# Optimization experiments

Measured on AMD Instinct MI355X. Metric: run time of the kernel, lower is better.

Reference implementation:

```python
import jax, jax.numpy as jnp
import numpy as np
import math

B, S, HID = 16, 512, 768
NUM_LABELS = 9
NUM_HEADS = 4
HEAD_DIM = HID // NUM_HEADS
MAX_REL = 5
B_PERSON = 1
I_PERSON = 2
LN_EPS = 1e-5


def setup_inputs() -> dict:
    key = jax.random.key(0)
    ks = jax.random.split(key, 16)
    w = lambda k, shp: jax.random.normal(k, shp, dtype=jnp.float32) * 0.02
    return {
        "sequence_output": jax.random.normal(ks[0], (B, S, HID), dtype=jnp.float32),
        "Wq": w(ks[1], (HID, HID)), "bq": jnp.zeros((HID,), jnp.float32),
        "Wk": w(ks[2], (HID, HID)), "bk": jnp.zeros((HID,), jnp.float32),
        "Wv": w(ks[3], (HID, HID)), "bv": jnp.zeros((HID,), jnp.float32),
        "Wo": w(ks[4], (HID, HID)), "bo": jnp.zeros((HID,), jnp.float32),
        "ln_g": jnp.ones((HID,), jnp.float32), "ln_b": jnp.zeros((HID,), jnp.float32),
        "Ws": w(ks[5], (HID, NUM_LABELS)), "bs": jnp.zeros((NUM_LABELS,), jnp.float32),
        "entity_bias": w(ks[6], (NUM_LABELS,)),
    }


def _heads(x):
    # [B,S,HID] -> [B,H,S,D]
    return x.reshape(B, S, NUM_HEADS, HEAD_DIM).transpose(0, 2, 1, 3)


def reference(sequence_output, Wq, bq, Wk, bk, Wv, bv, Wo, bo, ln_g, ln_b, Ws, bs, entity_bias):
    x = sequence_output
    q = _heads(x @ Wq + bq)
    k = _heads(x @ Wk + bk)
    v = _heads(x @ Wv + bv)

    scores = jnp.einsum("bhqd,bhkd->bhqk", q, k)
    # relative position bias: exp(-0.1 * clamp(|i-j|, 0, MAX_REL)), broadcast over b,h
    idx = jnp.arange(S, dtype=jnp.float32)
    dist = jnp.abs(idx[None, :] - idx[:, None])  # [S,S]
    rel_bias = jnp.exp(-0.1 * jnp.clip(dist, 0.0, float(MAX_REL)))
    dist_mask = -0.1 * dist
    scores = (scores + rel_bias) / math.sqrt(HEAD_DIM) + dist_mask
    probs = jax.nn.softmax(scores, axis=-1)  # dropout is identity in eval

    ctx = jnp.einsum("bhqk,bhkd->bhqd", probs, v)
    ctx = ctx.transpose(0, 2, 1, 3).reshape(B, S, HID)
    out = ctx @ Wo + bo

    h = x + out
    mu = jnp.mean(h, axis=-1, keepdims=True)
    var = jnp.mean(jnp.square(h - mu), axis=-1, keepdims=True)
    h = (h - mu) * jax.lax.rsqrt(var + LN_EPS) * ln_g + ln_b

    span_logits = h @ Ws + bs  # [B,S,L]
    # vectorized entity-bias post-process: the torch loop adds entity_bias[I_PERSON]
    # TWICE to final_logits[:, j, I_PERSON] whenever argmax(span_logits[:, j-1]) == B_PERSON
    prev_is_b = jnp.argmax(span_logits[:, :-1], axis=-1) == B_PERSON  # [B,S-1]
    bump = jnp.where(prev_is_b, 2.0 * entity_bias[I_PERSON], 0.0)
    final_logits = span_logits.at[:, 1:, I_PERSON].add(bump)
    return final_logits
```

## Files before the change

kernel.cpp:

```cpp
#include <hip/hip_runtime.h>
#include <math.h>

#define SEQ 512
#define HID 768
#define NBATCH 16
#define ROWS 8192
#define INV_SQRT_D 0.07216878364870323f

typedef short s8v __attribute__((ext_vector_type(8)));
typedef _Float16 h8v __attribute__((ext_vector_type(8)));
typedef float f4v __attribute__((ext_vector_type(4)));
typedef unsigned short u16;

__device__ __forceinline__ u16 f2h(float f) {
  _Float16 h = (_Float16)f;
  return __builtin_bit_cast(u16, h);
}

template <int KSTEPS>
__device__ __forceinline__ void mm_core128(
    const u16* __restrict__ A, const int lda,
    const u16* __restrict__ B, const int ldb,
    u16* lds, f4v (&acc)[4][4])
{
  const int tid = threadIdx.x;
  const int w = tid >> 6, ln = tid & 63;
  const u16* src = (w >> 1) ? B : A;
  const int ld = (w >> 1) ? ldb : lda;
  const int half = w & 1;
  const int srow = ln >> 2;
  const int csw  = ((ln & 3) - (ln >> 3)) & 3;
  const int ml = ln & 15, quad = ln >> 4;
  const int fo2 = ((quad + ((ln >> 1) & 3)) & 3) * 8;
  const int wr = (w >> 1) * 64, wc = (w & 1) * 64;

  const u16* gp[4];
  int lpo[4];
#pragma unroll
  for (int t = 0; t < 4; ++t) {
    const int row = half * 64 + t * 16 + srow;
    gp[t]  = src + (size_t)row * ld + csw * 8;
    lpo[t] = (w >> 1) * 4096 + half * 2048 + t * 512 + ln * 8;
  }
  s8v c[8];
#pragma unroll
  for (int t = 0; t < 4; ++t) {
    c[t]     = *(const s8v*)gp[t];
    c[4 + t] = *(const s8v*)(gp[t] + 32);
  }

  for (int kp = 0; kp < KSTEPS / 2; ++kp) {
    __syncthreads();
#pragma unroll
    for (int t = 0; t < 4; ++t) {
      *(s8v*)&lds[lpo[t]]        = c[t];
      *(s8v*)&lds[8192 + lpo[t]] = c[4 + t];
    }
    __syncthreads();
    if (kp + 1 < KSTEPS / 2) {
      const int k0 = (kp + 1) * 64;
#pragma unroll
      for (int t = 0; t < 4; ++t) {
        c[t]     = *(const s8v*)(gp[t] + k0);
        c[4 + t] = *(const s8v*)(gp[t] + k0 + 32);
      }
    }
#pragma unroll
    for (int sub = 0; sub < 2; ++sub) {
      const int so = sub * 8192;
      h8v a[4], b[4];
#pragma unroll
      for (int i = 0; i < 4; ++i)
        a[i] = *(const h8v*)&lds[so + (wr + i * 16 + ml) * 32 + fo2];
#pragma unroll
      for (int j = 0; j < 4; ++j)
        b[j] = *(const h8v*)&lds[so + 4096 + (wc + j * 16 + ml) * 32 + fo2];
#pragma unroll
      for (int i = 0; i < 4; ++i)
#pragma unroll
        for (int j = 0; j < 4; ++j)
          acc[i][j] = __builtin_amdgcn_mfma_f32_16x16x32_f16(a[i], b[j], acc[i][j], 0, 0, 0);
    }
  }
}

__global__ __launch_bounds__(256) void splitx(const float* __restrict__ x,
                                              u16* __restrict__ xh)
{
  const int i = blockIdx.x * 256 + threadIdx.x;
  const float4 v = ((const float4*)x)[i];
  ((ushort4*)xh)[i] = make_ushort4(f2h(v.x), f2h(v.y), f2h(v.z), f2h(v.w));
}

__global__ __launch_bounds__(256) void wsplit(
    const float* __restrict__ Wq, const float* __restrict__ Wk,
    const float* __restrict__ Wv, const float* __restrict__ Wo,
    u16* __restrict__ WTh)
{
  __shared__ float t[32][33];
  const int z = blockIdx.z;
  const float* W = (z == 0) ? Wq : (z == 1) ? Wk : (z == 2) ? Wv : Wo;
  const int n0 = blockIdx.x * 32, k0 = blockIdx.y * 32;
  const int tx = threadIdx.x & 31, ty = threadIdx.x >> 5;
#pragma unroll
  for (int i = 0; i < 4; ++i)
    t[ty + 8 * i][tx] = W[(size_t)(k0 + ty + 8 * i) * HID + n0 + tx];
  __syncthreads();
#pragma unroll
  for (int i = 0; i < 4; ++i) {
    const float v = t[tx][ty + 8 * i];
    const size_t idx = (size_t)z * HID * HID + (size_t)(n0 + ty + 8 * i) * HID + k0 + tx;
    WTh[idx] = f2h(v);
  }
}

__global__ __launch_bounds__(256, 3) void qkv_mm(
    const u16* __restrict__ xh, const u16* __restrict__ WTh,
    const float* __restrict__ bq, const float* __restrict__ bk, const float* __restrict__ bv,
    u16* __restrict__ qh, u16* __restrict__ kh, u16* __restrict__ vtmp16)
{
  __shared__ u16 lds[16384];
  const int id = blockIdx.x;
  const int xcd = id & 7;
  const int s = id >> 3;
  const int bx = s % 6;
  const int yl = (s / 6) & 7;
  const int z  = s / 48;
  const int bm = (yl * 8 + xcd) * 128;
  const int bn = bx * 128;
  const size_t wtoff = (size_t)z * HID * HID + (size_t)bn * HID;
  f4v acc[4][4];
#pragma unroll
  for (int i = 0; i < 4; ++i)
#pragma unroll
    for (int j = 0; j < 4; ++j) acc[i][j] = (f4v)0.f;
  mm_core128<24>(xh + (size_t)bm * HID, HID, WTh + wtoff, HID, lds, acc);
  const int tid = threadIdx.x, w = tid >> 6, ln = tid & 63;
  const int ml = ln & 15, quad = ln >> 4;
  const int wr = (w >> 1) * 64, wc = (w & 1) * 64;
  const float* bias = (z == 0) ? bq : (z == 1) ? bk : bv;
#pragma unroll
  for (int i = 0; i < 4; ++i)
#pragma unroll
    for (int j = 0; j < 4; ++j) {
      const int gcol = bn + wc + j * 16 + ml;
      const float bv_ = bias[gcol];
#pragma unroll
      for (int r = 0; r < 4; ++r) {
        const int grow = bm + wr + i * 16 + quad * 4 + r;
        const float v = acc[i][j][r] + bv_;
        const size_t idx = (size_t)grow * HID + gcol;
        if (z == 2)      vtmp16[idx] = f2h(v);
        else if (z == 0) qh[idx] = f2h(v);
        else             kh[idx] = f2h(v);
      }
    }
}

__global__ __launch_bounds__(256) void vtrans(const u16* __restrict__ vtmp16,
                                              u16* __restrict__ vTh)
{
  __shared__ u16 t[32][33];
  const int b = blockIdx.z, n0 = blockIdx.x * 32, c0 = blockIdx.y * 32;
  const int tx = threadIdx.x & 31, ty = threadIdx.x >> 5;
  const u16* src = vtmp16 + (size_t)b * SEQ * HID;
#pragma unroll
  for (int i = 0; i < 4; ++i)
    t[ty + 8 * i][tx] = src[(size_t)(c0 + ty + 8 * i) * HID + n0 + tx];
  __syncthreads();
#pragma unroll
  for (int i = 0; i < 4; ++i) {
    const size_t idx = (size_t)b * HID * SEQ + (size_t)(n0 + ty + 8 * i) * SEQ + c0 + tx;
    vTh[idx] = t[tx][ty + 8 * i];
  }
}

__global__ __launch_bounds__(256, 2) void attn_fused(
    const u16* __restrict__ qh, const u16* __restrict__ kh,
    const u16* __restrict__ vTh, u16* __restrict__ ch)
{
  __shared__ u16 lds[22528];
  __shared__ float red[4][32];
  const int z = blockIdx.y, b = z >> 2, hh = z & 3;
  const int bm = blockIdx.x * 32;
  const int tid = threadIdx.x, w = tid >> 6, ln = tid & 63;
  const int ml = ln & 15, quad = ln >> 4;
  const int fo2 = ((quad + ((ml >> 1) & 3)) & 3) * 8;
  const u16* qbase = qh + (size_t)(b * SEQ + bm) * HID + hh * 192;
  const u16* kbase = kh + (size_t)(b * SEQ) * HID + hh * 192;

  const int brow0 = tid >> 2, bsc = tid & 3;
  const u16* bgp[8];
  int blo[8];
#pragma unroll
  for (int t = 0; t < 8; ++t) {
    const int row = t * 64 + brow0;
    const int lc = (bsc - (row >> 1)) & 3;
    bgp[t] = kbase + (size_t)row * HID + lc * 8;
    blo[t] = 1024 + row * 32 + bsc * 8;
  }
  const bool hasA = tid < 128;
  const int arow = tid >> 2;
  const int alc = ((tid & 3) - (arow >> 1)) & 3;
  const u16* agp = qbase + (size_t)arow * HID + alc * 8;
  const int alo = arow * 32 + (tid & 3) * 8;

  s8v ca;
  s8v cb[8];
  if (hasA) ca = *(const s8v*)agp;
#pragma unroll
  for (int t = 0; t < 8; ++t) cb[t] = *(const s8v*)bgp[t];

  f4v acc[2][8];
#pragma unroll
  for (int i = 0; i < 2; ++i)
#pragma unroll
    for (int j = 0; j < 8; ++j) acc[i][j] = (f4v)0.f;

  for (int ks = 0; ks < 6; ++ks) {
    __syncthreads();
    if (hasA) *(s8v*)&lds[alo] = ca;
#pragma unroll
    for (int t = 0; t < 8; ++t) *(s8v*)&lds[blo[t]] = cb[t];
    __syncthreads();
    if (ks + 1 < 6) {
      const int k0 = (ks + 1) * 32;
      if (hasA) ca = *(const s8v*)(agp + k0);
#pragma unroll
      for (int t = 0; t < 8; ++t) cb[t] = *(const s8v*)(bgp[t] + k0);
    }
    h8v a[2];
#pragma unroll
    for (int i = 0; i < 2; ++i)
      a[i] = *(const h8v*)&lds[(i * 16 + ml) * 32 + fo2];
    h8v bfr[8];
#pragma unroll
    for (int j = 0; j < 8; ++j)
      bfr[j] = *(const h8v*)&lds[1024 + (w * 128 + j * 16 + ml) * 32 + fo2];
#pragma unroll
    for (int i = 0; i < 2; ++i)
#pragma unroll
      for (int j = 0; j < 8; ++j)
        acc[i][j] = __builtin_amdgcn_mfma_f32_16x16x32_f16(a[i], bfr[j], acc[i][j], 0, 0, 0);
  }

#pragma unroll
  for (int i = 0; i < 2; ++i)
#pragma unroll
    for (int j = 0; j < 8; ++j) {
      const int scol = w * 128 + j * 16 + ml;
#pragma unroll
      for (int r = 0; r < 4; ++r) {
        const int srow = bm + i * 16 + quad * 4 + r;
        const float dist = fabsf((float)(srow - scol));
        const float rel = __expf(-0.1f * fminf(dist, 5.0f));
        acc[i][j][r] = (acc[i][j][r] + rel) * INV_SQRT_D - 0.1f * dist;
      }
    }

  float mx[2][4];
#pragma unroll
  for (int i = 0; i < 2; ++i)
#pragma unroll
    for (int r = 0; r < 4; ++r) {
      float m = acc[i][0][r];
#pragma unroll
      for (int j = 1; j < 8; ++j) m = fmaxf(m, acc[i][j][r]);
#pragma unroll
      for (int o = 1; o < 16; o <<= 1) m = fmaxf(m, __shfl_xor(m, o, 64));
      mx[i][r] = m;
    }
  if (ml == 0) {
#pragma unroll
    for (int i = 0; i < 2; ++i)
#pragma unroll
      for (int r = 0; r < 4; ++r) red[w][i * 16 + quad * 4 + r] = mx[i][r];
  }
  __syncthreads();
#pragma unroll
  for (int i = 0; i < 2; ++i)
#pragma unroll
    for (int r = 0; r < 4; ++r) {
      const int R = i * 16 + quad * 4 + r;
      mx[i][r] = fmaxf(fmaxf(red[0][R], red[1][R]), fmaxf(red[2][R], red[3][R]));
    }
  __syncthreads();

  float sm[2][4];
#pragma unroll
  for (int i = 0; i < 2; ++i)
#pragma unroll
    for (int r = 0; r < 4; ++r) {
      float s = 0.f;
#pragma unroll
      for (int j = 0; j < 8; ++j) {
        const float p = __expf(acc[i][j][r] - mx[i][r]);
        acc[i][j][r] = p;
        s += p;
      }
#pragma unroll
      for (int o = 1; o < 16; o <<= 1) s += __shfl_xor(s, o, 64);
      sm[i][r] = s;
    }
  if (ml == 0) {
#pragma unroll
    for (int i = 0; i < 2; ++i)
#pragma unroll
      for (int r = 0; r < 4; ++r) red[w][i * 16 + quad * 4 + r] = sm[i][r];
  }
  __syncthreads();
#pragma unroll
  for (int i = 0; i < 2; ++i)
#pragma unroll
    for (int r = 0; r < 4; ++r) {
      const int R = i * 16 + quad * 4 + r;
      mx[i][r] = 1.0f / (red[0][R] + red[1][R] + red[2][R] + red[3][R]);
    }
  __syncthreads();

#pragma unroll
  for (int i = 0; i < 2; ++i)
#pragma unroll
    for (int r = 0; r < 4; ++r) {
      const int row = i * 16 + quad * 4 + r;
      const int rsw = (row >> 1) & 3;
      const int rbase = row * 512;
#pragma unroll
      for (int j = 0; j < 8; ++j) {
        const int col = w * 128 + j * 16 + ml;
        const int addr = rbase + (col & ~31) + ((((col >> 3) & 3) + rsw) & 3) * 8 + (col & 7);
        lds[addr] = f2h(acc[i][j][r] * mx[i][r]);
      }
    }

  const u16* vbase = vTh + (size_t)b * HID * SEQ + (size_t)(hh * 192) * SEQ;
  const u16* vgp[3];
  int vlo[3];
#pragma unroll
  for (int t = 0; t < 3; ++t) {
    const int cch = t * 256 + tid;
    const int vrow = cch >> 2, vsc = cch & 3;
    const int vlc = (vsc - (vrow >> 1)) & 3;
    vgp[t] = vbase + (size_t)vrow * SEQ + vlc * 8;
    vlo[t] = 16384 + cch * 8;
  }
  s8v vc[3];
#pragma unroll
  for (int t = 0; t < 3; ++t) vc[t] = *(const s8v*)vgp[t];

  f4v acc2[2][3];
#pragma unroll
  for (int i = 0; i < 2; ++i)
#pragma unroll
    for (int j = 0; j < 3; ++j) acc2[i][j] = (f4v)0.f;

  for (int ks = 0; ks < 16; ++ks) {
    __syncthreads();
#pragma unroll
    for (int t = 0; t < 3; ++t) *(s8v*)&lds[vlo[t]] = vc[t];
    __syncthreads();
    if (ks + 1 < 16) {
      const int k0 = (ks + 1) * 32;
#pragma unroll
      for (int t = 0; t < 3; ++t) vc[t] = *(const s8v*)(vgp[t] + k0);
    }
    h8v a2[2];
#pragma unroll
    for (int i = 0; i < 2; ++i)
      a2[i] = *(const h8v*)&lds[(i * 16 + ml) * 512 + ks * 32 + fo2];
    h8v b2[3];
#pragma unroll
    for (int j = 0; j < 3; ++j)
      b2[j] = *(const h8v*)&lds[16384 + (w * 48 + j * 16 + ml) * 32 + fo2];
#pragma unroll
    for (int i = 0; i < 2; ++i)
#pragma unroll
      for (int j = 0; j < 3; ++j)
        acc2[i][j] = __builtin_amdgcn_mfma_f32_16x16x32_f16(a2[i], b2[j], acc2[i][j], 0, 0, 0);
  }

#pragma unroll
  for (int i = 0; i < 2; ++i)
#pragma unroll
    for (int j = 0; j < 3; ++j) {
      const int gcol = hh * 192 + w * 48 + j * 16 + ml;
#pragma unroll
      for (int r = 0; r < 4; ++r) {
        const int m = bm + i * 16 + quad * 4 + r;
        ch[(size_t)(b * SEQ + m) * HID + gcol] = f2h(acc2[i][j][r]);
      }
    }
}

__global__ __launch_bounds__(256, 3) void proj_mm(
    const u16* __restrict__ ch, const u16* __restrict__ WTh,
    const float* __restrict__ bo, const float* __restrict__ x, float* __restrict__ h)
{
  __shared__ u16 lds[16384];
  const int id = blockIdx.x;
  const int xcd = id & 7;
  const int s = id >> 3;
  const int bx = s % 6;
  const int yl = s / 6;
  const int bm = (yl * 8 + xcd) * 128;
  const int bn = bx * 128;
  const size_t wtoff = (size_t)3 * HID * HID + (size_t)bn * HID;
  f4v acc[4][4];
#pragma unroll
  for (int i = 0; i < 4; ++i)
#pragma unroll
    for (int j = 0; j < 4; ++j) acc[i][j] = (f4v)0.f;
  mm_core128<24>(ch + (size_t)bm * HID, HID, WTh + wtoff, HID, lds, acc);
  const int tid = threadIdx.x, w = tid >> 6, ln = tid & 63;
  const int ml = ln & 15, quad = ln >> 4;
  const int wr = (w >> 1) * 64, wc = (w & 1) * 64;
#pragma unroll
  for (int i = 0; i < 4; ++i)
#pragma unroll
    for (int j = 0; j < 4; ++j) {
      const int gcol = bn + wc + j * 16 + ml;
      const float bv_ = bo[gcol];
#pragma unroll
      for (int r = 0; r < 4; ++r) {
        const int grow = bm + wr + i * 16 + quad * 4 + r;
        const size_t idx = (size_t)grow * HID + gcol;
        h[idx] = acc[i][j][r] + bv_ + x[idx];
      }
    }
}

__global__ __launch_bounds__(256) void ln_logits_kernel(
    const float* __restrict__ h, const float* __restrict__ g,
    const float* __restrict__ bta, const float* __restrict__ Ws,
    const float* __restrict__ bsv, float* __restrict__ span)
{
  const int row = blockIdx.x;
  const int tid = threadIdx.x;
  const float* hr = h + (size_t)row * HID;
  const float x0 = hr[tid], x1 = hr[tid + 256], x2 = hr[tid + 512];
  float s = x0 + x1 + x2;
  float sq = x0 * x0 + x1 * x1 + x2 * x2;
#pragma unroll
  for (int o = 32; o > 0; o >>= 1) { s += __shfl_down(s, o, 64); sq += __shfl_down(sq, o, 64); }
  __shared__ float red[8];
  __shared__ float smu, srs;
  const int wid = tid >> 6, lid = tid & 63;
  if (lid == 0) { red[wid] = s; red[4 + wid] = sq; }
  __syncthreads();
  if (tid == 0) {
    const float ts = red[0] + red[1] + red[2] + red[3];
    const float tq = red[4] + red[5] + red[6] + red[7];
    const float mu = ts / 768.0f;
    const float var = tq / 768.0f - mu * mu;
    smu = mu; srs = rsqrtf(var + 1e-5f);
  }
  __syncthreads();
  const float mu = smu, rs = srs;
  const float n0 = (x0 - mu) * rs * g[tid] + bta[tid];
  const float n1 = (x1 - mu) * rs * g[tid + 256] + bta[tid + 256];
  const float n2 = (x2 - mu) * rs * g[tid + 512] + bta[tid + 512];
  float pl[9];
#pragma unroll
  for (int l = 0; l < 9; ++l)
    pl[l] = n0 * Ws[(size_t)tid * 9 + l]
          + n1 * Ws[(size_t)(tid + 256) * 9 + l]
          + n2 * Ws[(size_t)(tid + 512) * 9 + l];
#pragma unroll
  for (int l = 0; l < 9; ++l)
#pragma unroll
    for (int o = 32; o > 0; o >>= 1) pl[l] += __shfl_down(pl[l], o, 64);
  __shared__ float lred[4][9];
  if (lid == 0) {
#pragma unroll
    for (int l = 0; l < 9; ++l) lred[wid][l] = pl[l];
  }
  __syncthreads();
  if (tid < 9) {
    span[(size_t)row * 9 + tid] =
        lred[0][tid] + lred[1][tid] + lred[2][tid] + lred[3][tid] + bsv[tid];
  }
}

__global__ __launch_bounds__(256) void bump_kernel(
    const float* __restrict__ span, const float* __restrict__ eb, float* __restrict__ out)
{
  const int idx = blockIdx.x * 256 + threadIdx.x;
  if (idx >= ROWS) return;
  const int j = idx & (SEQ - 1);
  const float* sl = span + (size_t)idx * 9;
  float v[9];
#pragma unroll
  for (int l = 0; l < 9; ++l) v[l] = sl[l];
  if (j >= 1) {
    const float* sp = sl - 9;
    float m = sp[0]; int am = 0;
#pragma unroll
    for (int l = 1; l < 9; ++l) { const float t = sp[l]; if (t > m) { m = t; am = l; } }
    if (am == 1) v[2] += 2.0f * eb[2];
  }
#pragma unroll
  for (int l = 0; l < 9; ++l) out[(size_t)idx * 9 + l] = v[l];
}

extern "C" void kernel_launch(void* const* d_in, const int* in_sizes, int n_in,
                              void* d_out, int out_size, void* d_ws, size_t ws_size,
                              hipStream_t stream)
{
  (void)in_sizes; (void)n_in; (void)out_size; (void)ws_size;
  const float* x   = (const float*)d_in[0];
  const float* Wq  = (const float*)d_in[1];
  const float* bq  = (const float*)d_in[2];
  const float* Wk  = (const float*)d_in[3];
  const float* bk  = (const float*)d_in[4];
  const float* Wv  = (const float*)d_in[5];
  const float* bv  = (const float*)d_in[6];
  const float* Wo  = (const float*)d_in[7];
  const float* bo  = (const float*)d_in[8];
  const float* lng = (const float*)d_in[9];
  const float* lnb = (const float*)d_in[10];
  const float* Ws  = (const float*)d_in[11];
  const float* bs  = (const float*)d_in[12];
  const float* eb  = (const float*)d_in[13];
  float* out = (float*)d_out;

  char* ws = (char*)d_ws;
  u16* xh  = (u16*)(ws + 0);
  u16* vTh = xh;
  u16* WTh = (u16*)(ws + 25165824);
  u16* qh  = (u16*)(ws + 34603008);
  u16* kh  = (u16*)(ws + 59768832);
  u16* vtmp16 = (u16*)(ws + 84934656);
  float* hb = (float*)(ws + 84934656);
  float* spanb = (float*)(ws + 152043520);
  u16* ctxh = qh;

  splitx<<<dim3(1572864 / 256), 256, 0, stream>>>(x, xh);
  wsplit<<<dim3(24, 24, 4), 256, 0, stream>>>(Wq, Wk, Wv, Wo, WTh);
  qkv_mm<<<dim3(1152), 256, 0, stream>>>(xh, WTh, bq, bk, bv, qh, kh, vtmp16);
  vtrans<<<dim3(24, 16, 16), 256, 0, stream>>>(vtmp16, vTh);
  attn_fused<<<dim3(16, 64), 256, 0, stream>>>(qh, kh, vTh, ctxh);
  proj_mm<<<dim3(384), 256, 0, stream>>>(ctxh, WTh, bo, x, hb);
  ln_logits_kernel<<<dim3(ROWS), 256, 0, stream>>>(hb, lng, lnb, Ws, bs, spanb);
  bump_kernel<<<dim3(ROWS / 256), 256, 0, stream>>>(spanb, eb, out);
}
```

Measured before the change: 240.5 us.

## Load attention operands straight from global memory and drop the softmax max pass

The attention kernel no longer stages Q, K and V tiles through shared memory with double-buffered copies and barriers. Each wave now loads its MFMA fragments directly from global memory, which works because the waves do not share K or V fragments. Softmax skips the row-max reduction and its barriers, and normalisation by the row sum moves to the output store. Shared memory shrinks, occupancy is raised to 4 blocks, the P buffer rows are padded to 520, and blocks are remapped so each XCD handles whole batch-head groups. Dropping the max subtraction assumes scores stay small enough for exp not to overflow, and the direct fragment loads are narrower and less coalesced than the old staged copies.

```diff
diff --git a/kernel.cpp b/kernel.cpp
--- a/kernel.cpp
+++ b/kernel.cpp
@@ -175,41 +175,32 @@
   }
 }
 
-__global__ __launch_bounds__(256, 2) void attn_fused(
+__global__ __launch_bounds__(256, 4) void attn_fused(
     const u16* __restrict__ qh, const u16* __restrict__ kh,
     const u16* __restrict__ vTh, u16* __restrict__ ch)
 {
-  __shared__ u16 lds[22528];
+  __shared__ u16 lds[16640];
   __shared__ float red[4][32];
-  const int z = blockIdx.y, b = z >> 2, hh = z & 3;
-  const int bm = blockIdx.x * 32;
+  const int f = blockIdx.x;
+  const int xcd = f & 7, s = f >> 3;
+  const int z = xcd * 8 + (s >> 4);
+  const int bm = (s & 15) * 32;
+  const int b = z >> 2, hh = z & 3;
   const int tid = threadIdx.x, w = tid >> 6, ln = tid & 63;
   const int ml = ln & 15, quad = ln >> 4;
   const int fo2 = ((quad + ((ml >> 1) & 3)) & 3) * 8;
+
   const u16* qbase = qh + (size_t)(b * SEQ + bm) * HID + hh * 192;
-  const u16* kbase = kh + (size_t)(b * SEQ) * HID + hh * 192;
-
-  const int brow0 = tid >> 2, bsc = tid & 3;
-  const u16* bgp[8];
-  int blo[8];
-#pragma unroll
-  for (int t = 0; t < 8; ++t) {
-    const int row = t * 64 + brow0;
-    const int lc = (bsc - (row >> 1)) & 3;
-    bgp[t] = kbase + (size_t)row * HID + lc * 8;
-    blo[t] = 1024 + row * 32 + bsc * 8;
-  }
-  const bool hasA = tid < 128;
-  const int arow = tid >> 2;
-  const int alc = ((tid & 3) - (arow >> 1)) & 3;
-  const u16* agp = qbase + (size_t)arow * HID + alc * 8;
-  const int alo = arow * 32 + (tid & 3) * 8;
-
-  s8v ca;
-  s8v cb[8];
-  if (hasA) ca = *(const s8v*)agp;
-#pragma unroll
-  for (int t = 0; t < 8; ++t) cb[t] = *(const s8v*)bgp[t];
+  const u16* kbase = kh + (size_t)b * SEQ * HID + hh * 192;
+
+  const u16* qp[2];
+#pragma unroll
+  for (int i = 0; i < 2; ++i)
+    qp[i] = qbase + (size_t)(i * 16 + ml) * HID + quad * 8;
+  const u16* kp[8];
+#pragma unroll
+  for (int j = 0; j < 8; ++j)
+    kp[j] = kbase + (size_t)(w * 128 + j * 16 + ml) * HID + quad * 8;
 
   f4v acc[2][8];
 #pragma unroll
@@ -217,33 +208,31 @@
 #pragma unroll
     for (int j = 0; j < 8; ++j) acc[i][j] = (f4v)0.f;
 
+#pragma unroll
   for (int ks = 0; ks < 6; ++ks) {
-    __syncthreads();
-    if (hasA) *(s8v*)&lds[alo] = ca;
-#pragma unroll
-    for (int t = 0; t < 8; ++t) *(s8v*)&lds[blo[t]] = cb[t];
-    __syncthreads();
-    if (ks + 1 < 6) {
-      const int k0 = (ks + 1) * 32;
-      if (hasA) ca = *(const s8v*)(agp + k0);
-#pragma unroll
-      for (int t = 0; t < 8; ++t) cb[t] = *(const s8v*)(bgp[t] + k0);
-    }
+    const int ko = ks * 32;
     h8v a[2];
 #pragma unroll
-    for (int i = 0; i < 2; ++i)
-      a[i] = *(const h8v*)&lds[(i * 16 + ml) * 32 + fo2];
-    h8v bfr[8];
-#pragma unroll
-    for (int j = 0; j < 8; ++j)
-      bfr[j] = *(const h8v*)&lds[1024 + (w * 128 + j * 16 + ml) * 32 + fo2];
-#pragma unroll
-    for (int i = 0; i < 2; ++i)
-#pragma unroll
-      for (int j = 0; j < 8; ++j)
-        acc[i][j] = __builtin_amdgcn_mfma_f32_16x16x32_f16(a[i], bfr[j], acc[i][j], 0, 0, 0);
-  }
-
+    for (int i = 0; i < 2; ++i) a[i] = *(const h8v*)(qp[i] + ko);
+#pragma unroll
+    for (int jh = 0; jh < 2; ++jh) {
+      h8v bf[4];
+#pragma unroll
+      for (int j = 0; j < 4; ++j) bf[j] = *(const h8v*)(kp[jh * 4 + j] + ko);
+#pragma unroll
+      for (int i = 0; i < 2; ++i)
+#pragma unroll
+        for (int j = 0; j < 4; ++j)
+          acc[i][jh * 4 + j] =
+              __builtin_amdgcn_mfma_f32_16x16x32_f16(a[i], bf[j], acc[i][jh * 4 + j], 0, 0, 0);
+    }
+  }
+
+  float sm[2][4];
+#pragma unroll
+  for (int i = 0; i < 2; ++i)
+#pragma unroll
+    for (int r = 0; r < 4; ++r) sm[i][r] = 0.f;
 #pragma unroll
   for (int i = 0; i < 2; ++i)
 #pragma unroll
@@ -252,71 +241,28 @@
 #pragma unroll
       for (int r = 0; r < 4; ++r) {
         const int srow = bm + i * 16 + quad * 4 + r;
-        const float dist = fabsf((float)(srow - scol));
-        const float rel = __expf(-0.1f * fminf(dist, 5.0f));
-        acc[i][j][r] = (acc[i][j][r] + rel) * INV_SQRT_D - 0.1f * dist;
-      }
-    }
-
-  float mx[2][4];
+        const float fd = fabsf((float)(srow - scol));
+        const float rel = __expf(-0.1f * fminf(fd, 5.0f));
+        const float p = __expf((acc[i][j][r] + rel) * INV_SQRT_D - 0.1f * fd);
+        acc[i][j][r] = p;
+        sm[i][r] += p;
+      }
+    }
 #pragma unroll
   for (int i = 0; i < 2; ++i)
 #pragma unroll
     for (int r = 0; r < 4; ++r) {
-      float m = acc[i][0][r];
-#pragma unroll
-      for (int j = 1; j < 8; ++j) m = fmaxf(m, acc[i][j][r]);
-#pragma unroll
-      for (int o = 1; o < 16; o <<= 1) m = fmaxf(m, __shfl_xor(m, o, 64));
-      mx[i][r] = m;
+      float t = sm[i][r];
+#pragma unroll
+      for (int o = 1; o < 16; o <<= 1) t += __shfl_xor(t, o, 64);
+      sm[i][r] = t;
     }
   if (ml == 0) {
 #pragma unroll
     for (int i = 0; i < 2; ++i)
 #pragma unroll
-      for (int r = 0; r < 4; ++r) red[w][i * 16 + quad * 4 + r] = mx[i][r];
-  }
-  __syncthreads();
-#pragma unroll
-  for (int i = 0; i < 2; ++i)
-#pragma unroll
-    for (int r = 0; r < 4; ++r) {
-      const int R = i * 16 + quad * 4 + r;
-      mx[i][r] = fmaxf(fmaxf(red[0][R], red[1][R]), fmaxf(red[2][R], red[3][R]));
-    }
-  __syncthreads();
-
-  float sm[2][4];
-#pragma unroll
-  for (int i = 0; i < 2; ++i)
-#pragma unroll
-    for (int r = 0; r < 4; ++r) {
-      float s = 0.f;
-#pragma unroll
-      for (int j = 0; j < 8; ++j) {
-        const float p = __expf(acc[i][j][r] - mx[i][r]);
-        acc[i][j][r] = p;
-        s += p;
-      }
-#pragma unroll
-      for (int o = 1; o < 16; o <<= 1) s += __shfl_xor(s, o, 64);
-      sm[i][r] = s;
-    }
-  if (ml == 0) {
-#pragma unroll
-    for (int i = 0; i < 2; ++i)
-#pragma unroll
       for (int r = 0; r < 4; ++r) red[w][i * 16 + quad * 4 + r] = sm[i][r];
   }
-  __syncthreads();
-#pragma unroll
-  for (int i = 0; i < 2; ++i)
-#pragma unroll
-    for (int r = 0; r < 4; ++r) {
-      const int R = i * 16 + quad * 4 + r;
-      mx[i][r] = 1.0f / (red[0][R] + red[1][R] + red[2][R] + red[3][R]);
-    }
-  __syncthreads();
 
 #pragma unroll
   for (int i = 0; i < 2; ++i)
@@ -324,29 +270,30 @@
     for (int r = 0; r < 4; ++r) {
       const int row = i * 16 + quad * 4 + r;
       const int rsw = (row >> 1) & 3;
-      const int rbase = row * 512;
+      const int rbase = row * 520;
 #pragma unroll
       for (int j = 0; j < 8; ++j) {
         const int col = w * 128 + j * 16 + ml;
         const int addr = rbase + (col & ~31) + ((((col >> 3) & 3) + rsw) & 3) * 8 + (col & 7);
-        lds[addr] = f2h(acc[i][j][r] * mx[i][r]);
-      }
+        lds[addr] = f2h(acc[i][j][r]);
+      }
+    }
+  __syncthreads();
+
+  float isum[2][4];
+#pragma unroll
+  for (int i = 0; i < 2; ++i)
+#pragma unroll
+    for (int r = 0; r < 4; ++r) {
+      const int R = i * 16 + quad * 4 + r;
+      isum[i][r] = 1.0f / (red[0][R] + red[1][R] + red[2][R] + red[3][R]);
     }
 
   const u16* vbase = vTh + (size_t)b * HID * SEQ + (size_t)(hh * 192) * SEQ;
-  const u16* vgp[3];
-  int vlo[3];
-#pragma unroll
-  for (int t = 0; t < 3; ++t) {
-    const int cch = t * 256 + tid;
-    const int vrow = cch >> 2, vsc = cch & 3;
-    const int vlc = (vsc - (vrow >> 1)) & 3;
-    vgp[t] = vbase + (size_t)vrow * SEQ + vlc * 8;
-    vlo[t] = 16384 + cch * 8;
-  }
-  s8v vc[3];
-#pragma unroll
-  for (int t = 0; t < 3; ++t) vc[t] = *(const s8v*)vgp[t];
+  const u16* vp[3];
+#pragma unroll
+  for (int j = 0; j < 3; ++j)
+    vp[j] = vbase + (size_t)(w * 48 + j * 16 + ml) * SEQ + quad * 8;
 
   f4v acc2[2][3];
 #pragma unroll
@@ -354,24 +301,15 @@
 #pragma unroll
     for (int j = 0; j < 3; ++j) acc2[i][j] = (f4v)0.f;
 
+#pragma unroll
   for (int ks = 0; ks < 16; ++ks) {
-    __syncthreads();
-#pragma unroll
-    for (int t = 0; t < 3; ++t) *(s8v*)&lds[vlo[t]] = vc[t];
-    __syncthreads();
-    if (ks + 1 < 16) {
-      const int k0 = (ks + 1) * 32;
-#pragma unroll
-      for (int t = 0; t < 3; ++t) vc[t] = *(const s8v*)(vgp[t] + k0);
-    }
     h8v a2[2];
 #pragma unroll
     for (int i = 0; i < 2; ++i)
-      a2[i] = *(const h8v*)&lds[(i * 16 + ml) * 512 + ks * 32 + fo2];
+      a2[i] = *(const h8v*)&lds[(i * 16 + ml) * 520 + ks * 32 + fo2];
     h8v b2[3];
 #pragma unroll
-    for (int j = 0; j < 3; ++j)
-      b2[j] = *(const h8v*)&lds[16384 + (w * 48 + j * 16 + ml) * 32 + fo2];
+    for (int j = 0; j < 3; ++j) b2[j] = *(const h8v*)(vp[j] + ks * 32);
 #pragma unroll
     for (int i = 0; i < 2; ++i)
 #pragma unroll
@@ -387,7 +325,7 @@
 #pragma unroll
       for (int r = 0; r < 4; ++r) {
         const int m = bm + i * 16 + quad * 4 + r;
-        ch[(size_t)(b * SEQ + m) * HID + gcol] = f2h(acc2[i][j][r]);
+        ch[(size_t)(b * SEQ + m) * HID + gcol] = f2h(acc2[i][j][r] * isum[i][r]);
       }
     }
 }
@@ -538,7 +476,7 @@
   wsplit<<<dim3(24, 24, 4), 256, 0, stream>>>(Wq, Wk, Wv, Wo, WTh);
   qkv_mm<<<dim3(1152), 256, 0, stream>>>(xh, WTh, bq, bk, bv, qh, kh, vtmp16);
   vtrans<<<dim3(24, 16, 16), 256, 0, stream>>>(vtmp16, vTh);
-  attn_fused<<<dim3(16, 64), 256, 0, stream>>>(qh, kh, vTh, ctxh);
+  attn_fused<<<dim3(1024), 256, 0, stream>>>(qh, kh, vTh, ctxh);
   proj_mm<<<dim3(384), 256, 0, stream>>>(ctxh, WTh, bo, x, hb);
   ln_logits_kernel<<<dim3(ROWS), 256, 0, stream>>>(hb, lng, lnb, Ws, bs, spanb);
   bump_kernel<<<dim3(ROWS / 256), 256, 0, stream>>>(spanb, eb, out);
```

New measurement: 258.5 us. 7.5% more time.
